# Performance work log

Hardware: AMD Instinct MI355X
Metric: run time of the kernel (lower is better)

Reference implementation:

```python
import jax, jax.numpy as jnp
import numpy as np

D, T, B, DEPTH, WIN, H = 1024, 2048, 4, 2, 128, 4
HD = D // H


def setup_inputs() -> dict:
    key = jax.random.key(0)
    ks = iter(jax.random.split(key, 32))
    s = D ** -0.5
    inp = {
        'x': jax.random.normal(next(ks), (B, T, D), jnp.float32),
        'ln1_s': jnp.ones((DEPTH, D)), 'ln1_b': jnp.zeros((DEPTH, D)),
        'ln2_s': jnp.ones((DEPTH, D)), 'ln2_b': jnp.zeros((DEPTH, D)),
        'ln3_s': jnp.ones((DEPTH, D)), 'ln3_b': jnp.zeros((DEPTH, D)),
        'rg_in_w': jax.random.normal(next(ks), (DEPTH, D, D)) * s,
        'rg_in_b': jnp.zeros((DEPTH, D)),
        'rg_gate_w': jax.random.normal(next(ks), (DEPTH, D, D)) * s,
        'rg_gate_b': jnp.zeros((DEPTH, D)),
        'rg_out_w': jax.random.normal(next(ks), (DEPTH, D, D)) * s,
        'rg_out_b': jnp.zeros((DEPTH, D)),
        'qkv_w': jax.random.normal(next(ks), (DEPTH, D, 3 * D)) * s,
        'qkv_b': jnp.zeros((DEPTH, 3 * D)),
        'attn_out_w': jax.random.normal(next(ks), (DEPTH, D, D)) * s,
        'attn_out_b': jnp.zeros((DEPTH, D)),
        'mlp_w1': jax.random.normal(next(ks), (DEPTH, D, 4 * D)) * s,
        'mlp_b1': jnp.zeros((DEPTH, 4 * D)),
        'mlp_w2': jax.random.normal(next(ks), (DEPTH, 4 * D, D)) * (4 * D) ** -0.5,
        'mlp_b2': jnp.zeros((DEPTH, D)),
    }
    return inp


def _ln(x, s, b):
    m = x.mean(-1, keepdims=True)
    v = ((x - m) ** 2).mean(-1, keepdims=True)
    return (x - m) / jnp.sqrt(v + 1e-5) * s + b


def _rg_lru(x, wi, bi, wg, bg, wo, bo):
    u = x @ wi + bi                      # [B,T,D]
    g = jax.nn.sigmoid(x @ wg + bg)      # [B,T,D]
    # h_t = g_t * h_{t-1} + (1-g_t) * u_t, h_{-1}=0 -> log-depth associative scan
    def comb(l, r):
        return (l[0] * r[0], r[0] * l[1] + r[1])
    _, h = jax.lax.associative_scan(comb, (g, (1.0 - g) * u), axis=1)
    return h @ wo + bo


def _local_attn(x, wqkv, bqkv, wo, bo):
    b, t, d = x.shape
    qkv = (x @ wqkv + bqkv).reshape(b, t, 3, H, HD)
    qkv = jnp.transpose(qkv, (2, 0, 3, 1, 4))  # [3,B,H,T,hd]
    q, k, v = qkv[0], qkv[1], qkv[2]
    scores = jnp.einsum('bhid,bhjd->bhij', q, k) / (HD ** 0.5)
    i = jnp.arange(t)[:, None]
    j = jnp.arange(t)[None, :]
    mask = (j <= i) & (j >= i - (WIN - 1))
    scores = jnp.where(mask, scores, -jnp.inf)
    p = jax.nn.softmax(scores, axis=-1)
    y = jnp.einsum('bhij,bhjd->bhid', p, v)
    y = jnp.transpose(y, (0, 2, 1, 3)).reshape(b, t, d)
    return y @ wo + bo


def reference(x, ln1_s, ln1_b, ln2_s, ln2_b, ln3_s, ln3_b,
              rg_in_w, rg_in_b, rg_gate_w, rg_gate_b, rg_out_w, rg_out_b,
              qkv_w, qkv_b, attn_out_w, attn_out_b,
              mlp_w1, mlp_b1, mlp_w2, mlp_b2):
    for l in range(DEPTH):
        x = x + _rg_lru(_ln(x, ln1_s[l], ln1_b[l]),
                        rg_in_w[l], rg_in_b[l], rg_gate_w[l], rg_gate_b[l],
                        rg_out_w[l], rg_out_b[l])
        x = x + _local_attn(_ln(x, ln2_s[l], ln2_b[l]),
                            qkv_w[l], qkv_b[l], attn_out_w[l], attn_out_b[l])
        h = _ln(x, ln3_s[l], ln3_b[l])
        h = jax.nn.gelu(h @ mlp_w1[l] + mlp_b1[l], approximate=False) @ mlp_w2[l] + mlp_b2[l]
        x = x + h
    return x
```

## Files before the change

### kernel.cpp

```cpp
#include <hip/hip_runtime.h>
#include <math.h>

#define DD 1024
#define TT 2048
#define BB 4
#define HH 4
#define HDIM 256
#define NLAYER 2
#define MM (BB*TT)
#define NCHUNK 32
#define CHUNK (TT/NCHUNK)

typedef unsigned short u16;
typedef __bf16 bf16x8 __attribute__((ext_vector_type(8)));
typedef float f32x4 __attribute__((ext_vector_type(4)));

__device__ __forceinline__ float b2f(u16 h) {
  unsigned u = ((unsigned)h) << 16;
  return __builtin_bit_cast(float, u);
}
__device__ __forceinline__ u16 f2b(float f) {
  unsigned u = __builtin_bit_cast(unsigned, f);
  u += 0x7fffu + ((u >> 16) & 1u);
  return (u16)(u >> 16);
}
__device__ __forceinline__ float blo(unsigned u) { return __builtin_bit_cast(float, u << 16); }
__device__ __forceinline__ float bhi(unsigned u) { return __builtin_bit_cast(float, u & 0xffff0000u); }

#define GLD16(g, l) __builtin_amdgcn_global_load_lds( \
    (__attribute__((address_space(1))) void*)(void*)(g), \
    (__attribute__((address_space(3))) void*)(l), 16, 0, 0)

__device__ __forceinline__ void wg_barrier() {
  asm volatile("" ::: "memory");
  __builtin_amdgcn_s_barrier();
  asm volatile("" ::: "memory");
}

__global__ __launch_bounds__(256)
void transpose_cvt(const float* __restrict__ W, u16* __restrict__ Wt, int K, int N) {
  __shared__ float tile[32][33];
  const int n0 = blockIdx.x << 5, k0 = blockIdx.y << 5;
  const int tx = threadIdx.x, ty = threadIdx.y;
#pragma unroll
  for (int i = 0; i < 4; ++i)
    tile[ty + i*8][tx] = W[(size_t)(k0 + ty + i*8) * N + n0 + tx];
  __syncthreads();
#pragma unroll
  for (int i = 0; i < 4; ++i)
    Wt[(size_t)(n0 + ty + i*8) * K + k0 + tx] = f2b(tile[tx][ty + i*8]);
}

__global__ __launch_bounds__(256)
void ln_k(const float* __restrict__ x, const float* __restrict__ sc,
          const float* __restrict__ bi, u16* __restrict__ xn) {
  const int row = blockIdx.x;
  const int tid = threadIdx.x;
  const float4 xv = ((const float4*)(x + (size_t)row * DD))[tid];
  float s = xv.x + xv.y + xv.z + xv.w;
  float q = xv.x*xv.x + xv.y*xv.y + xv.z*xv.z + xv.w*xv.w;
#pragma unroll
  for (int o = 1; o < 64; o <<= 1) { s += __shfl_xor(s, o); q += __shfl_xor(q, o); }
  __shared__ float rs[4], rq[4];
  if ((tid & 63) == 0) { rs[tid >> 6] = s; rq[tid >> 6] = q; }
  __syncthreads();
  s = rs[0] + rs[1] + rs[2] + rs[3];
  q = rq[0] + rq[1] + rq[2] + rq[3];
  const float mean = s * (1.f / DD);
  const float var = q * (1.f / DD) - mean * mean;
  const float rstd = rsqrtf(var + 1e-5f);
  const float4 sv = ((const float4*)sc)[tid];
  const float4 bv = ((const float4*)bi)[tid];
  const u16 o0 = f2b((xv.x - mean) * rstd * sv.x + bv.x);
  const u16 o1 = f2b((xv.y - mean) * rstd * sv.y + bv.y);
  const u16 o2 = f2b((xv.z - mean) * rstd * sv.z + bv.z);
  const u16 o3 = f2b((xv.w - mean) * rstd * sv.w + bv.w);
  uint2 pk;
  pk.x = (unsigned)o0 | ((unsigned)o1 << 16);
  pk.y = (unsigned)o2 | ((unsigned)o3 << 16);
  *(uint2*)(xn + (size_t)row * DD + (tid << 2)) = pk;
}

template<int EPI>
__global__ __launch_bounds__(256)
void gemm_k(const u16* __restrict__ A, const u16* __restrict__ Wt,
            const float* __restrict__ bias, const float* __restrict__ bias2,
            float* __restrict__ outf, float* __restrict__ outf2,
            u16* __restrict__ outb, int K, int N) {
  __shared__ u16 As[2][8192];
  __shared__ u16 Bs[2][8192];
  const int tid = threadIdx.x;
  const int gx = gridDim.x;
  const int nwg = gx * (int)gridDim.y;
  int lid = (int)blockIdx.y * gx + (int)blockIdx.x;
  lid = (lid & 7) * (nwg >> 3) + (lid >> 3);
  const int m0 = (lid / gx) << 7;
  const int n0 = (lid % gx) << 7;
  const int lane = tid & 63;
  const int wm = (tid >> 7) & 1;
  const int wn = (tid >> 6) & 1;
  const int g = lane >> 4;
  const int lc = lane & 15;
  const int sw = lc & 7;
  const int rowst = tid >> 3;
  const int aslot = (tid & 7) ^ (rowst & 7);

  const u16* Abase = A  + (size_t)m0 * K;
  const u16* Bbase = Wt + (size_t)n0 * K;

  auto stage = [&](int kt, int buf) {
    const int ko = (kt << 6) + (aslot << 3);
#pragma unroll
    for (int i = 0; i < 4; ++i) {
      GLD16(Abase + (size_t)(i*32 + rowst) * K + ko, As[buf] + (i*256 + tid)*8);
      GLD16(Bbase + (size_t)(i*32 + rowst) * K + ko, Bs[buf] + (i*256 + tid)*8);
    }
  };

  f32x4 acc[4][4];
#pragma unroll
  for (int i = 0; i < 4; ++i)
#pragma unroll
    for (int j = 0; j < 4; ++j)
#pragma unroll
      for (int e = 0; e < 4; ++e) acc[i][j][e] = 0.f;

  const int KT = K >> 6;
  stage(0, 0);
  stage(1, 1);
  for (int kt = 0; kt < KT; ++kt) {
    const int cur = kt & 1;
    if (kt + 1 < KT) asm volatile("s_waitcnt vmcnt(8)" ::: "memory");
    else             asm volatile("s_waitcnt vmcnt(0)" ::: "memory");
    __builtin_amdgcn_s_barrier();
    asm volatile("" ::: "memory");
    const u16* Ac = As[cur];
    const u16* Bc = Bs[cur];
#pragma unroll
    for (int kk = 0; kk < 2; ++kk) {
      const int ko = ((kk*4 + g) ^ sw) << 3;
      bf16x8 af[4], bfr[4];
#pragma unroll
      for (int mi = 0; mi < 4; ++mi)
        af[mi] = *(const bf16x8*)(Ac + ((wm*64 + mi*16 + lc) << 6) + ko);
#pragma unroll
      for (int ni = 0; ni < 4; ++ni)
        bfr[ni] = *(const bf16x8*)(Bc + ((wn*64 + ni*16 + lc) << 6) + ko);
      __builtin_amdgcn_s_setprio(1);
#pragma unroll
      for (int mi = 0; mi < 4; ++mi)
#pragma unroll
        for (int ni = 0; ni < 4; ++ni)
          acc[mi][ni] = __builtin_amdgcn_mfma_f32_16x16x32_bf16(af[mi], bfr[ni], acc[mi][ni], 0, 0, 0);
      __builtin_amdgcn_s_setprio(0);
    }
    wg_barrier();
    if (kt + 2 < KT) stage(kt + 2, cur);
  }

#pragma unroll
  for (int mi = 0; mi < 4; ++mi) {
#pragma unroll
    for (int ni = 0; ni < 4; ++ni) {
      const int n = n0 + (wn << 6) + ni*16 + lc;
      const int mbase = m0 + (wm << 6) + mi*16 + (g << 2);
      if (EPI == 4) {
        const float bia = bias[n];
        if (n < 2048) {
#pragma unroll
          for (int e = 0; e < 4; ++e)
            outb[(size_t)(mbase + e) * 2048 + n] = f2b(acc[mi][ni][e] + bia);
        } else {
          const int hh = (n - 2048) >> 8, dim = (n - 2048) & 255;
          const int bidx = mbase >> 11, t = mbase & 2047;
          const u16 a0 = f2b(acc[mi][ni][0] + bia);
          const u16 a1 = f2b(acc[mi][ni][1] + bia);
          const u16 a2 = f2b(acc[mi][ni][2] + bia);
          const u16 a3 = f2b(acc[mi][ni][3] + bia);
          uint2 pk;
          pk.x = (unsigned)a0 | ((unsigned)a1 << 16);
          pk.y = (unsigned)a2 | ((unsigned)a3 << 16);
          u16* vtp = (u16*)outf;
          *(uint2*)(vtp + ((size_t)((bidx*4 + hh)*256 + dim)) * 2048 + t) = pk;
        }
      } else if (EPI == 5) {
        const float bia = (n < 1024) ? bias[n] : bias2[n - 1024];
        u16* dst = (n < 1024) ? (u16*)outf : (u16*)outf2;
        const int nn = n & 1023;
#pragma unroll
        for (int e = 0; e < 4; ++e)
          dst[(size_t)(mbase + e) * 1024 + nn] = f2b(acc[mi][ni][e] + bia);
      } else {
        const float bia = bias[n];
#pragma unroll
        for (int e = 0; e < 4; ++e) {
          const float v = acc[mi][ni][e] + bia;
          const size_t idx = (size_t)(mbase + e) * N + n;
          if (EPI == 2) {
            const float zc = fminf(fmaxf(1.5957691216f * (v + 0.044715f*v*v*v), -30.f), 30.f);
            outb[idx] = f2b(v / (1.f + __expf(-zc)));
          } else outf[idx] += v;
        }
      }
    }
  }
}

__global__ __launch_bounds__(256)
void scan1_k(const u16* __restrict__ zpre, const u16* __restrict__ u,
             float* __restrict__ aggA, float* __restrict__ aggB) {
  const int d = blockIdx.x * 256 + threadIdx.x;
  const int c = blockIdx.y, b = blockIdx.z;
  const size_t base = ((size_t)b * TT + (size_t)c * CHUNK) * DD + d;
  float a = 1.f, acc = 0.f;
  for (int t = 0; t < CHUNK; ++t) {
    const float gl = 1.f / (1.f + __expf(-b2f(zpre[base + (size_t)t * DD])));
    const float ul = b2f(u[base + (size_t)t * DD]);
    acc = gl * acc + (1.f - gl) * ul;
    a *= gl;
  }
  const size_t o = ((size_t)b * NCHUNK + c) * DD + d;
  aggA[o] = a; aggB[o] = acc;
}

__global__ __launch_bounds__(256)
void scan2_k(const float* __restrict__ aggA, const float* __restrict__ aggB,
             float* __restrict__ carry) {
  const int idx = blockIdx.x * 256 + threadIdx.x;
  const int b = idx >> 10, d = idx & 1023;
  float h = 0.f;
  for (int c = 0; c < NCHUNK; ++c) {
    const size_t o = ((size_t)b * NCHUNK + c) * DD + d;
    carry[o] = h;
    h = aggA[o] * h + aggB[o];
  }
}

__global__ __launch_bounds__(256)
void scan3_k(const u16* __restrict__ zpre, const u16* __restrict__ u,
             const float* __restrict__ carry, u16* __restrict__ hout) {
  const int d = blockIdx.x * 256 + threadIdx.x;
  const int c = blockIdx.y, b = blockIdx.z;
  const size_t base = ((size_t)b * TT + (size_t)c * CHUNK) * DD + d;
  float h = carry[((size_t)b * NCHUNK + c) * DD + d];
  for (int t = 0; t < CHUNK; ++t) {
    const float gl = 1.f / (1.f + __expf(-b2f(zpre[base + (size_t)t * DD])));
    const float ul = b2f(u[base + (size_t)t * DD]);
    h = gl * h + (1.f - gl) * ul;
    hout[base + (size_t)t * DD] = f2b(h);
  }
}

__global__ __launch_bounds__(256)
void attn_mfma(const u16* __restrict__ qkb, const u16* __restrict__ vt,
               u16* __restrict__ y) {
  __shared__ u16 kv[16384];
  __shared__ u16 pb[4][16][200];
  const int tid = threadIdx.x;
  const int lane = tid & 63;
  const int wid = tid >> 6;
  const int g = lane >> 4;
  const int lc = lane & 15;
  const int t0 = blockIdx.x << 6;
  const int bh = blockIdx.y;
  const int bT = (bh >> 2) * TT;
  const int h = bh & 3;

  bf16x8 afq[8];
  {
    const u16* qg = qkb + (size_t)(bT + t0 + wid*16 + lc) * 2048 + h*256 + g*8;
#pragma unroll
    for (int ks = 0; ks < 8; ++ks)
      afq[ks] = __builtin_bit_cast(bf16x8, *(const uint4*)(qg + ks*32));
  }

  f32x4 sc[12];
#pragma unroll
  for (int f = 0; f < 12; ++f)
#pragma unroll
    for (int e = 0; e < 4; ++e) sc[f][e] = 0.f;

  const int koff = 1024 + h*256;
#pragma unroll
  for (int c = 0; c < 3; ++c) {
    const int j0 = t0 + (c - 2) * 64;
    if (j0 < 0) {
#pragma unroll
      for (int nt = 0; nt < 4; ++nt)
#pragma unroll
        for (int e = 0; e < 4; ++e) sc[c*4+nt][e] = -1e30f;
      continue;
    }
    __syncthreads();
    {
      const u16* kg = qkb + (size_t)(bT + j0) * 2048 + koff;
#pragma unroll
      for (int i = 0; i < 8; ++i) {
        const int o16 = i*256 + tid;
        const int slab = o16 >> 8, key = (o16 >> 2) & 63, ds = o16 & 3;
        GLD16(kg + (size_t)key*2048 + slab*32 + ds*8, kv + o16*8);
      }
    }
    __syncthreads();
#pragma unroll
    for (int nt = 0; nt < 4; ++nt) {
      f32x4 s = sc[c*4+nt];
#pragma unroll
      for (int ks = 0; ks < 8; ++ks) {
        const bf16x8 kb = *(const bf16x8*)(kv + ks*2048 + (nt*16 + lc)*32 + g*8);
        s = __builtin_amdgcn_mfma_f32_16x16x32_bf16(afq[ks], kb, s, 0, 0, 0);
      }
      sc[c*4+nt] = s;
    }
#pragma unroll
    for (int nt = 0; nt < 4; ++nt)
#pragma unroll
      for (int e = 0; e < 4; ++e) {
        const int tl = wid*16 + g*4 + e;
        const int jl = nt*16 + lc;
        const bool ok = (c == 1) || (c == 2 ? (jl <= tl) : (jl >= tl + 1));
        sc[c*4+nt][e] = ok ? sc[c*4+nt][e] * 0.0625f : -1e30f;
      }
  }

#pragma unroll
  for (int e = 0; e < 4; ++e) {
    float m = -1e30f;
#pragma unroll
    for (int f = 0; f < 12; ++f) m = fmaxf(m, sc[f][e]);
    m = fmaxf(m, __shfl_xor(m, 1)); m = fmaxf(m, __shfl_xor(m, 2));
    m = fmaxf(m, __shfl_xor(m, 4)); m = fmaxf(m, __shfl_xor(m, 8));
    float s = 0.f;
#pragma unroll
    for (int f = 0; f < 12; ++f) { const float p = __expf(sc[f][e] - m); sc[f][e] = p; s += p; }
    s += __shfl_xor(s, 1); s += __shfl_xor(s, 2);
    s += __shfl_xor(s, 4); s += __shfl_xor(s, 8);
    const float is = 1.f / s;
#pragma unroll
    for (int f = 0; f < 12; ++f) sc[f][e] *= is;
  }
#pragma unroll
  for (int c = 0; c < 3; ++c)
#pragma unroll
    for (int nt = 0; nt < 4; ++nt)
#pragma unroll
      for (int e = 0; e < 4; ++e)
        pb[wid][g*4 + e][c*64 + nt*16 + lc] = f2b(sc[c*4+nt][e]);

  f32x4 acc[16];
#pragma unroll
  for (int nt = 0; nt < 16; ++nt)
#pragma unroll
    for (int e = 0; e < 4; ++e) acc[nt][e] = 0.f;

  const u16* vg = vt + (size_t)bh * 256 * 2048;
#pragma unroll
  for (int c = 0; c < 3; ++c) {
    const int j0 = t0 + (c - 2) * 64;
    if (j0 < 0) continue;
    __syncthreads();
#pragma unroll
    for (int i = 0; i < 8; ++i) {
      const int o16 = i*256 + tid;
      const int dim = o16 >> 3, slot = o16 & 7;
      const int ss = slot ^ (dim & 7);
      GLD16(vg + (size_t)dim*2048 + j0 + ss*8, kv + o16*8);
    }
    __syncthreads();
#pragma unroll
    for (int ks = 0; ks < 2; ++ks) {
      const bf16x8 pa = *(const bf16x8*)&pb[wid][lc][(c*2 + ks)*32 + g*8];
#pragma unroll
      for (int nt = 0; nt < 16; ++nt) {
        const int dim = nt*16 + lc;
        int boff = dim*128 + ks*64 + g*16;
        boff ^= (dim & 7) << 4;
        const bf16x8 vb = *(const bf16x8*)((const char*)kv + boff);
        acc[nt] = __builtin_amdgcn_mfma_f32_16x16x32_bf16(pa, vb, acc[nt], 0, 0, 0);
      }
    }
  }

#pragma unroll
  for (int nt = 0; nt < 16; ++nt)
#pragma unroll
    for (int e = 0; e < 4; ++e) {
      const int tok = bT + t0 + wid*16 + g*4 + e;
      y[(size_t)tok * 1024 + h*256 + nt*16 + lc] = f2b(acc[nt][e]);
    }
}

extern "C" void kernel_launch(void* const* d_in, const int* in_sizes, int n_in,
                              void* d_out, int out_size, void* d_ws, size_t ws_size,
                              hipStream_t stream) {
  const float* x_in      = (const float*)d_in[0];
  const float* ln1_s     = (const float*)d_in[1];
  const float* ln1_b     = (const float*)d_in[2];
  const float* ln2_s     = (const float*)d_in[3];
  const float* ln2_b     = (const float*)d_in[4];
  const float* ln3_s     = (const float*)d_in[5];
  const float* ln3_b     = (const float*)d_in[6];
  const float* rg_in_w   = (const float*)d_in[7];
  const float* rg_in_b   = (const float*)d_in[8];
  const float* rg_gate_w = (const float*)d_in[9];
  const float* rg_gate_b = (const float*)d_in[10];
  const float* rg_out_w  = (const float*)d_in[11];
  const float* rg_out_b  = (const float*)d_in[12];
  const float* qkv_w     = (const float*)d_in[13];
  const float* qkv_b     = (const float*)d_in[14];
  const float* attn_out_w= (const float*)d_in[15];
  const float* attn_out_b= (const float*)d_in[16];
  const float* mlp_w1    = (const float*)d_in[17];
  const float* mlp_b1    = (const float*)d_in[18];
  const float* mlp_w2    = (const float*)d_in[19];
  const float* mlp_b2    = (const float*)d_in[20];

  float* x = (float*)d_out;
  char* ws = (char*)d_ws;
  u16*  wt     = (u16*)ws;
  u16*  xn     = (u16*)(ws + 62914560);
  char* bigS   = ws + 62914560 + 16777216;
  char* smallS = bigS + 67108864;
  float* aggA  = (float*)(smallS + 16777216);
  float* aggB  = aggA + (size_t)BB * NCHUNK * DD;
  float* carry = aggB + (size_t)BB * NCHUNK * DD;

  u16* ubuf = (u16*)bigS;
  u16* zbuf = (u16*)(bigS + 33554432);
  u16* qkb  = (u16*)bigS;
  u16* vtb  = (u16*)(bigS + 33554432);
  u16* hid  = (u16*)bigS;
  u16* hbuf = (u16*)smallS;
  u16* ybuf = (u16*)smallS;

  hipMemcpyAsync(x, x_in, (size_t)MM * DD * sizeof(float), hipMemcpyDeviceToDevice, stream);

  const size_t LW = 15728640;
  const dim3 tb(32, 8);
  for (int l = 0; l < NLAYER; ++l) {
    u16* base = wt + (size_t)l * LW;
    transpose_cvt<<<dim3(32, 32),  tb, 0, stream>>>(rg_in_w   + (size_t)l*DD*DD,   base + 0,        DD, DD);
    transpose_cvt<<<dim3(32, 32),  tb, 0, stream>>>(rg_gate_w + (size_t)l*DD*DD,   base + 1048576,  DD, DD);
    transpose_cvt<<<dim3(32, 32),  tb, 0, stream>>>(rg_out_w  + (size_t)l*DD*DD,   base + 2097152,  DD, DD);
    transpose_cvt<<<dim3(96, 32),  tb, 0, stream>>>(qkv_w     + (size_t)l*DD*3072, base + 3145728,  DD, 3072);
    transpose_cvt<<<dim3(32, 32),  tb, 0, stream>>>(attn_out_w+ (size_t)l*DD*DD,   base + 6291456,  DD, DD);
    transpose_cvt<<<dim3(128, 32), tb, 0, stream>>>(mlp_w1    + (size_t)l*DD*4096, base + 7340032,  DD, 4096);
    transpose_cvt<<<dim3(32, 128), tb, 0, stream>>>(mlp_w2    + (size_t)l*4096*DD, base + 11534336, 4096, DD);
  }

  for (int l = 0; l < NLAYER; ++l) {
    u16* base = wt + (size_t)l * LW;
    ln_k<<<MM, 256, 0, stream>>>(x, ln1_s + l*DD, ln1_b + l*DD, xn);
    gemm_k<5><<<dim3(16, 64), 256, 0, stream>>>(xn, base + 0, rg_in_b + l*DD, rg_gate_b + l*DD,
                                                (float*)ubuf, (float*)zbuf, nullptr, DD, 2048);
    scan1_k<<<dim3(4, NCHUNK, BB), 256, 0, stream>>>(zbuf, ubuf, aggA, aggB);
    scan2_k<<<16, 256, 0, stream>>>(aggA, aggB, carry);
    scan3_k<<<dim3(4, NCHUNK, BB), 256, 0, stream>>>(zbuf, ubuf, carry, hbuf);
    gemm_k<3><<<dim3(8, 64), 256, 0, stream>>>(hbuf, base + 2097152, rg_out_b + l*DD, nullptr,
                                               x, nullptr, nullptr, DD, DD);
    ln_k<<<MM, 256, 0, stream>>>(x, ln2_s + l*DD, ln2_b + l*DD, xn);
    gemm_k<4><<<dim3(24, 64), 256, 0, stream>>>(xn, base + 3145728, qkv_b + l*3072, nullptr,
                                                (float*)vtb, nullptr, qkb, DD, 3072);
    attn_mfma<<<dim3(TT/64, BB*HH), 256, 0, stream>>>(qkb, vtb, ybuf);
    gemm_k<3><<<dim3(8, 64), 256, 0, stream>>>(ybuf, base + 6291456, attn_out_b + l*DD, nullptr,
                                               x, nullptr, nullptr, DD, DD);
    ln_k<<<MM, 256, 0, stream>>>(x, ln3_s + l*DD, ln3_b + l*DD, xn);
    gemm_k<2><<<dim3(32, 64), 256, 0, stream>>>(xn, base + 7340032, mlp_b1 + l*4096, nullptr,
                                                nullptr, nullptr, hid, DD, 4096);
    gemm_k<3><<<dim3(8, 64), 256, 0, stream>>>(hid, base + 11534336, mlp_b2 + l*DD, nullptr,
                                               x, nullptr, nullptr, 4096, DD);
  }
}
```

Before: 945.4 us.

## Add 256x256-tile GEMM kernel with 8 waves for wide-N projections

Adds a new 512-thread GEMM kernel with 256x256 output tiles and 128KB of dynamic LDS. Global loads of the next K-tile are split into four parts and interleaved with the MFMA sub-steps of the current tile. It is used for the wide projections (RG-LRU in/gate, QKV, MLP up). The goal is higher arithmetic intensity and less global/L2 traffic per FLOP than the 128x128 kernel. In exchange it uses more registers and LDS, has fewer workgroups per CU, and launches fewer tiles, which can hurt occupancy and wave balance on 256 CUs.

```diff
diff --git a/kernel.cpp b/kernel.cpp
--- a/kernel.cpp
+++ b/kernel.cpp
@@ -82,11 +82,144 @@
 }
 
 template<int EPI>
+__global__ __launch_bounds__(512, 2)
+void gemm256_k(const u16* __restrict__ A, const u16* __restrict__ Wt,
+               const float* __restrict__ bias, const float* __restrict__ bias2,
+               float* __restrict__ outf, u16* __restrict__ outb, int K, int N) {
+  extern __shared__ u16 lds[];
+  u16* Al = lds;
+  u16* Bl = lds + 32768;
+  const int tid = threadIdx.x;
+  const int gx = gridDim.x;
+  const int nwg = gx * (int)gridDim.y;
+  int lid = (int)blockIdx.y * gx + (int)blockIdx.x;
+  lid = (lid & 7) * (nwg >> 3) + (lid >> 3);
+  const int m0 = (lid / gx) << 8;
+  const int n0 = (lid % gx) << 8;
+  const int lane = tid & 63;
+  const int wid = tid >> 6;
+  const int wm = wid >> 2;
+  const int wn = wid & 3;
+  const int g = lane >> 4;
+  const int lc = lane & 15;
+
+  const int srow = tid >> 3;
+  const int sslot = tid & 7;
+
+  auto stage_part = [&](int kt, int c, int p) {
+    if (p < 2) {
+#pragma unroll
+      for (int i = p*2; i < p*2 + 2; ++i) {
+        const int row = i*64 + srow;
+        GLD16(A + (size_t)(m0 + row) * K + kt*64 + ((sslot ^ (row & 7)) << 3),
+              Al + c*16384 + row*64 + sslot*8);
+      }
+    } else {
+#pragma unroll
+      for (int i = (p-2)*2; i < (p-2)*2 + 2; ++i) {
+        const int row = i*64 + srow;
+        GLD16(Wt + (size_t)(n0 + row) * K + kt*64 + ((sslot ^ (row & 7)) << 3),
+              Bl + c*16384 + row*64 + sslot*8);
+      }
+    }
+  };
+
+  f32x4 acc[8][4];
+#pragma unroll
+  for (int i = 0; i < 8; ++i)
+#pragma unroll
+    for (int j = 0; j < 4; ++j)
+#pragma unroll
+      for (int e = 0; e < 4; ++e) acc[i][j][e] = 0.f;
+
+  const int KT = K >> 6;
+#pragma unroll
+  for (int p = 0; p < 4; ++p) stage_part(0, 0, p);
+
+  for (int kt = 0; kt < KT; ++kt) {
+    const int cur = kt & 1;
+    asm volatile("s_waitcnt vmcnt(0)" ::: "memory");
+    wg_barrier();
+    bf16x8 bfr[4];
+#pragma unroll
+    for (int p = 0; p < 4; ++p) {
+      const int kk = p >> 1, mh = p & 1;
+      const int c16 = ((kk*4 + g) ^ (lc & 7)) << 3;
+      bf16x8 af[4];
+#pragma unroll
+      for (int i = 0; i < 4; ++i) {
+        const int row = wm*128 + (mh*4 + i)*16 + lc;
+        af[i] = *(const bf16x8*)(Al + cur*16384 + row*64 + c16);
+      }
+      if (mh == 0) {
+#pragma unroll
+        for (int ni = 0; ni < 4; ++ni) {
+          const int row = wn*64 + ni*16 + lc;
+          bfr[ni] = *(const bf16x8*)(Bl + cur*16384 + row*64 + c16);
+        }
+      }
+      if (kt + 1 < KT) stage_part(kt + 1, cur ^ 1, p);
+      wg_barrier();
+      __builtin_amdgcn_s_setprio(1);
+#pragma unroll
+      for (int i = 0; i < 4; ++i)
+#pragma unroll
+        for (int ni = 0; ni < 4; ++ni)
+          acc[mh*4 + i][ni] = __builtin_amdgcn_mfma_f32_16x16x32_bf16(af[i], bfr[ni], acc[mh*4 + i][ni], 0, 0, 0);
+      __builtin_amdgcn_s_setprio(0);
+      wg_barrier();
+    }
+  }
+
+#pragma unroll
+  for (int mi = 0; mi < 8; ++mi) {
+#pragma unroll
+    for (int ni = 0; ni < 4; ++ni) {
+      const int n = n0 + wn*64 + ni*16 + lc;
+      const int mbase = m0 + wm*128 + mi*16 + (g << 2);
+      if (EPI == 4) {
+        const float bia = bias[n];
+        if (n < 2048) {
+#pragma unroll
+          for (int e = 0; e < 4; ++e)
+            outb[(size_t)(mbase + e) * 2048 + n] = f2b(acc[mi][ni][e] + bia);
+        } else {
+          const int hh = (n - 2048) >> 8, dim = (n - 2048) & 255;
+          const int bidx = mbase >> 11, t = mbase & 2047;
+          const u16 a0 = f2b(acc[mi][ni][0] + bia);
+          const u16 a1 = f2b(acc[mi][ni][1] + bia);
+          const u16 a2 = f2b(acc[mi][ni][2] + bia);
+          const u16 a3 = f2b(acc[mi][ni][3] + bia);
+          uint2 pk;
+          pk.x = (unsigned)a0 | ((unsigned)a1 << 16);
+          pk.y = (unsigned)a2 | ((unsigned)a3 << 16);
+          u16* vtp = (u16*)outf;
+          *(uint2*)(vtp + ((size_t)((bidx*4 + hh)*256 + dim)) * 2048 + t) = pk;
+        }
+      } else if (EPI == 5) {
+        const float bia = (n < 1024) ? bias[n] : bias2[n - 1024];
+        u16* dst = (n < 1024) ? outb : (u16*)outf;
+        const int nn = n & 1023;
+#pragma unroll
+        for (int e = 0; e < 4; ++e)
+          dst[(size_t)(mbase + e) * 1024 + nn] = f2b(acc[mi][ni][e] + bia);
+      } else {
+        const float bia = bias[n];
+#pragma unroll
+        for (int e = 0; e < 4; ++e) {
+          const float v = acc[mi][ni][e] + bia;
+          const float zc = fminf(fmaxf(1.5957691216f * (v + 0.044715f*v*v*v), -30.f), 30.f);
+          outb[(size_t)(mbase + e) * N + n] = f2b(v / (1.f + __expf(-zc)));
+        }
+      }
+    }
+  }
+}
+
+template<int EPI>
 __global__ __launch_bounds__(256)
 void gemm_k(const u16* __restrict__ A, const u16* __restrict__ Wt,
-            const float* __restrict__ bias, const float* __restrict__ bias2,
-            float* __restrict__ outf, float* __restrict__ outf2,
-            u16* __restrict__ outb, int K, int N) {
+            const float* __restrict__ bias, float* __restrict__ outf, int K, int N) {
   __shared__ u16 As[2][8192];
   __shared__ u16 Bs[2][8192];
   const int tid = threadIdx.x;
@@ -164,44 +297,10 @@
     for (int ni = 0; ni < 4; ++ni) {
       const int n = n0 + (wn << 6) + ni*16 + lc;
       const int mbase = m0 + (wm << 6) + mi*16 + (g << 2);
-      if (EPI == 4) {
-        const float bia = bias[n];
-        if (n < 2048) {
-#pragma unroll
-          for (int e = 0; e < 4; ++e)
-            outb[(size_t)(mbase + e) * 2048 + n] = f2b(acc[mi][ni][e] + bia);
-        } else {
-          const int hh = (n - 2048) >> 8, dim = (n - 2048) & 255;
-          const int bidx = mbase >> 11, t = mbase & 2047;
-          const u16 a0 = f2b(acc[mi][ni][0] + bia);
-          const u16 a1 = f2b(acc[mi][ni][1] + bia);
-          const u16 a2 = f2b(acc[mi][ni][2] + bia);
-          const u16 a3 = f2b(acc[mi][ni][3] + bia);
-          uint2 pk;
-          pk.x = (unsigned)a0 | ((unsigned)a1 << 16);
-          pk.y = (unsigned)a2 | ((unsigned)a3 << 16);
-          u16* vtp = (u16*)outf;
-          *(uint2*)(vtp + ((size_t)((bidx*4 + hh)*256 + dim)) * 2048 + t) = pk;
-        }
-      } else if (EPI == 5) {
-        const float bia = (n < 1024) ? bias[n] : bias2[n - 1024];
-        u16* dst = (n < 1024) ? (u16*)outf : (u16*)outf2;
-        const int nn = n & 1023;
-#pragma unroll
-        for (int e = 0; e < 4; ++e)
-          dst[(size_t)(mbase + e) * 1024 + nn] = f2b(acc[mi][ni][e] + bia);
-      } else {
-        const float bia = bias[n];
-#pragma unroll
-        for (int e = 0; e < 4; ++e) {
-          const float v = acc[mi][ni][e] + bia;
-          const size_t idx = (size_t)(mbase + e) * N + n;
-          if (EPI == 2) {
-            const float zc = fminf(fmaxf(1.5957691216f * (v + 0.044715f*v*v*v), -30.f), 30.f);
-            outb[idx] = f2b(v / (1.f + __expf(-zc)));
-          } else outf[idx] += v;
-        }
-      }
+      const float bia = bias[n];
+#pragma unroll
+      for (int e = 0; e < 4; ++e)
+        outf[(size_t)(mbase + e) * N + n] += acc[mi][ni][e] + bia;
     }
   }
 }
@@ -415,6 +514,10 @@
   const float* mlp_w2    = (const float*)d_in[19];
   const float* mlp_b2    = (const float*)d_in[20];
 
+  hipFuncSetAttribute((const void*)&gemm256_k<5>, hipFuncAttributeMaxDynamicSharedMemorySize, 131072);
+  hipFuncSetAttribute((const void*)&gemm256_k<4>, hipFuncAttributeMaxDynamicSharedMemorySize, 131072);
+  hipFuncSetAttribute((const void*)&gemm256_k<2>, hipFuncAttributeMaxDynamicSharedMemorySize, 131072);
+
   float* x = (float*)d_out;
   char* ws = (char*)d_ws;
   u16*  wt     = (u16*)ws;
@@ -451,23 +554,20 @@
   for (int l = 0; l < NLAYER; ++l) {
     u16* base = wt + (size_t)l * LW;
     ln_k<<<MM, 256, 0, stream>>>(x, ln1_s + l*DD, ln1_b + l*DD, xn);
-    gemm_k<5><<<dim3(16, 64), 256, 0, stream>>>(xn, base + 0, rg_in_b + l*DD, rg_gate_b + l*DD,
-                                                (float*)ubuf, (float*)zbuf, nullptr, DD, 2048);
+    gemm256_k<5><<<dim3(8, 32), 512, 131072, stream>>>(xn, base + 0, rg_in_b + l*DD, rg_gate_b + l*DD,
+                                                       (float*)zbuf, ubuf, DD, 2048);
     scan1_k<<<dim3(4, NCHUNK, BB), 256, 0, stream>>>(zbuf, ubuf, aggA, aggB);
     scan2_k<<<16, 256, 0, stream>>>(aggA, aggB, carry);
     scan3_k<<<dim3(4, NCHUNK, BB), 256, 0, stream>>>(zbuf, ubuf, carry, hbuf);
-    gemm_k<3><<<dim3(8, 64), 256, 0, stream>>>(hbuf, base + 2097152, rg_out_b + l*DD, nullptr,
-                                               x, nullptr, nullptr, DD, DD);
+    gemm_k<3><<<dim3(8, 64), 256, 0, stream>>>(hbuf, base + 2097152, rg_out_b + l*DD, x, DD, DD);
     ln_k<<<MM, 256, 0, stream>>>(x, ln2_s + l*DD, ln2_b + l*DD, xn);
-    gemm_k<4><<<dim3(24, 64), 256, 0, stream>>>(xn, base + 3145728, qkv_b + l*3072, nullptr,
-                                                (float*)vtb, nullptr, qkb, DD, 3072);
+    gemm256_k<4><<<dim3(12, 32), 512, 131072, stream>>>(xn, base + 3145728, qkv_b + l*3072, nullptr,
+                                                        (float*)vtb, qkb, DD, 3072);
     attn_mfma<<<dim3(TT/64, BB*HH), 256, 0, stream>>>(qkb, vtb, ybuf);
-    gemm_k<3><<<dim3(8, 64), 256, 0, stream>>>(ybuf, base + 6291456, attn_out_b + l*DD, nullptr,
-                                               x, nullptr, nullptr, DD, DD);
+    gemm_k<3><<<dim3(8, 64), 256, 0, stream>>>(ybuf, base + 6291456, attn_out_b + l*DD, x, DD, DD);
     ln_k<<<MM, 256, 0, stream>>>(x, ln3_s + l*DD, ln3_b + l*DD, xn);
-    gemm_k<2><<<dim3(32, 64), 256, 0, stream>>>(xn, base + 7340032, mlp_b1 + l*4096, nullptr,
-                                                nullptr, nullptr, hid, DD, 4096);
-    gemm_k<3><<<dim3(8, 64), 256, 0, stream>>>(hid, base + 11534336, mlp_b2 + l*DD, nullptr,
-                                               x, nullptr, nullptr, 4096, DD);
-  }
-}
+    gemm256_k<2><<<dim3(16, 32), 512, 131072, stream>>>(xn, base + 7340032, mlp_b1 + l*4096, nullptr,
+                                                        nullptr, hid, DD, 4096);
+    gemm_k<3><<<dim3(8, 64), 256, 0, stream>>>(hid, base + 11534336, mlp_b2 + l*DD, x, 4096, DD);
+  }
+}
```

Result: faster. 920.3 us (-2.6%).

## Replace 128x128 GEMM with 256-row, 512-thread tiles and split-K staging

Applied to the files above, without the earlier changes.

Swaps the 128x128 bf16 MFMA GEMM for a 256xBN tile (BN 256 or 128) run by 8 waves, using dynamic LDS up to 128KB. Each 64-wide k-step is staged as two 32-wide halves, and the next tile's loads are issued mid-iteration instead of keeping a fixed two-ahead prefetch. The aim is more reuse per LDS load and fewer blocks. In exchange it needs more registers and LDS per block, which lowers occupancy, and leaves small grids (256 blocks) for the N=1024 GEMMs.

```diff
diff --git a/kernel.cpp b/kernel.cpp
--- a/kernel.cpp
+++ b/kernel.cpp
@@ -24,8 +24,6 @@
   u += 0x7fffu + ((u >> 16) & 1u);
   return (u16)(u >> 16);
 }
-__device__ __forceinline__ float blo(unsigned u) { return __builtin_bit_cast(float, u << 16); }
-__device__ __forceinline__ float bhi(unsigned u) { return __builtin_bit_cast(float, u & 0xffff0000u); }
 
 #define GLD16(g, l) __builtin_amdgcn_global_load_lds( \
     (__attribute__((address_space(1))) void*)(void*)(g), \
@@ -35,6 +33,9 @@
   asm volatile("" ::: "memory");
   __builtin_amdgcn_s_barrier();
   asm volatile("" ::: "memory");
+}
+template<int N> __device__ __forceinline__ void wait_vmcnt() {
+  asm volatile("s_waitcnt vmcnt(%0)" :: "i"(N) : "memory");
 }
 
 __global__ __launch_bounds__(256)
@@ -81,89 +82,112 @@
   *(uint2*)(xn + (size_t)row * DD + (tid << 2)) = pk;
 }
 
-template<int EPI>
-__global__ __launch_bounds__(256)
-void gemm_k(const u16* __restrict__ A, const u16* __restrict__ Wt,
-            const float* __restrict__ bias, const float* __restrict__ bias2,
-            float* __restrict__ outf, float* __restrict__ outf2,
-            u16* __restrict__ outb, int K, int N) {
-  __shared__ u16 As[2][8192];
-  __shared__ u16 Bs[2][8192];
+template<int EPI, int BN>
+__global__ __launch_bounds__(512)
+void gemm256t(const u16* __restrict__ A, const u16* __restrict__ Wt,
+              const float* __restrict__ bias, const float* __restrict__ bias2,
+              float* __restrict__ outf, u16* __restrict__ outb, int K, int N) {
+  constexpr int NI = BN / 64;
+  constexpr int PAIR = 2 + BN / 128;
+  extern __shared__ u16 lds[];
+  u16* Al = lds;
+  u16* Bl = lds + 32768;
   const int tid = threadIdx.x;
   const int gx = gridDim.x;
   const int nwg = gx * (int)gridDim.y;
   int lid = (int)blockIdx.y * gx + (int)blockIdx.x;
   lid = (lid & 7) * (nwg >> 3) + (lid >> 3);
-  const int m0 = (lid / gx) << 7;
-  const int n0 = (lid % gx) << 7;
+  const int m0 = (lid / gx) << 8;
+  const int n0 = (lid % gx) * BN;
   const int lane = tid & 63;
-  const int wm = (tid >> 7) & 1;
-  const int wn = (tid >> 6) & 1;
+  const int wid = tid >> 6;
+  const int wm = wid >> 2;
+  const int wn = wid & 3;
   const int g = lane >> 4;
   const int lc = lane & 15;
-  const int sw = lc & 7;
-  const int rowst = tid >> 3;
-  const int aslot = (tid & 7) ^ (rowst & 7);
-
-  const u16* Abase = A  + (size_t)m0 * K;
-  const u16* Bbase = Wt + (size_t)n0 * K;
-
-  auto stage = [&](int kt, int buf) {
-    const int ko = (kt << 6) + (aslot << 3);
-#pragma unroll
-    for (int i = 0; i < 4; ++i) {
-      GLD16(Abase + (size_t)(i*32 + rowst) * K + ko, As[buf] + (i*256 + tid)*8);
-      GLD16(Bbase + (size_t)(i*32 + rowst) * K + ko, Bs[buf] + (i*256 + tid)*8);
+  const int rkey = (lc >> 1) & 3;
+  const int q = tid >> 2;
+  const int sslot = tid & 3;
+  const int skey = (q >> 1) & 3;
+  const int scs = (sslot ^ skey) << 3;
+
+  auto stage_pair = [&](int kt, int buf, int ch) {
+    const int kbase = (kt << 6) + (ch << 5);
+#pragma unroll
+    for (int i = 0; i < 2; ++i) {
+      const int row = i*128 + q;
+      GLD16(A + (size_t)(m0 + row) * K + kbase + scs,
+            Al + buf*16384 + ch*8192 + i*4096 + tid*8);
+    }
+#pragma unroll
+    for (int i = 0; i < BN/128; ++i) {
+      const int row = i*128 + q;
+      GLD16(Wt + (size_t)(n0 + row) * K + kbase + scs,
+            Bl + buf*(BN*64) + ch*(BN*32) + i*4096 + tid*8);
     }
   };
 
-  f32x4 acc[4][4];
-#pragma unroll
-  for (int i = 0; i < 4; ++i)
-#pragma unroll
-    for (int j = 0; j < 4; ++j)
+  f32x4 acc[8][NI];
+#pragma unroll
+  for (int i = 0; i < 8; ++i)
+#pragma unroll
+    for (int j = 0; j < NI; ++j)
 #pragma unroll
       for (int e = 0; e < 4; ++e) acc[i][j][e] = 0.f;
 
   const int KT = K >> 6;
-  stage(0, 0);
-  stage(1, 1);
+  stage_pair(0, 0, 0);
+  stage_pair(0, 0, 1);
+
   for (int kt = 0; kt < KT; ++kt) {
     const int cur = kt & 1;
-    if (kt + 1 < KT) asm volatile("s_waitcnt vmcnt(8)" ::: "memory");
-    else             asm volatile("s_waitcnt vmcnt(0)" ::: "memory");
-    __builtin_amdgcn_s_barrier();
-    asm volatile("" ::: "memory");
-    const u16* Ac = As[cur];
-    const u16* Bc = Bs[cur];
+    const bool more = (kt + 1 < KT);
 #pragma unroll
     for (int kk = 0; kk < 2; ++kk) {
-      const int ko = ((kk*4 + g) ^ sw) << 3;
-      bf16x8 af[4], bfr[4];
-#pragma unroll
-      for (int mi = 0; mi < 4; ++mi)
-        af[mi] = *(const bf16x8*)(Ac + ((wm*64 + mi*16 + lc) << 6) + ko);
-#pragma unroll
-      for (int ni = 0; ni < 4; ++ni)
-        bfr[ni] = *(const bf16x8*)(Bc + ((wn*64 + ni*16 + lc) << 6) + ko);
+      if (kk == 0) wait_vmcnt<PAIR>();
+      else if (more) wait_vmcnt<PAIR>();
+      else wait_vmcnt<0>();
+      wg_barrier();
+      const int so = (g ^ rkey) << 3;
+      const u16* Ab = Al + cur*16384 + kk*8192;
+      const u16* Bb = Bl + cur*(BN*64) + kk*(BN*32);
+      bf16x8 bfr[NI];
+#pragma unroll
+      for (int ni = 0; ni < NI; ++ni)
+        bfr[ni] = *(const bf16x8*)(Bb + (wn*(NI*16) + ni*16 + lc)*32 + so);
+      bf16x8 af0[4];
+#pragma unroll
+      for (int i = 0; i < 4; ++i)
+        af0[i] = *(const bf16x8*)(Ab + (wm*128 + i*16 + lc)*32 + so);
+      if (more) stage_pair(kt + 1, cur ^ 1, kk);
       __builtin_amdgcn_s_setprio(1);
 #pragma unroll
-      for (int mi = 0; mi < 4; ++mi)
-#pragma unroll
-        for (int ni = 0; ni < 4; ++ni)
-          acc[mi][ni] = __builtin_amdgcn_mfma_f32_16x16x32_bf16(af[mi], bfr[ni], acc[mi][ni], 0, 0, 0);
+      for (int i = 0; i < 4; ++i)
+#pragma unroll
+        for (int ni = 0; ni < NI; ++ni)
+          acc[i][ni] = __builtin_amdgcn_mfma_f32_16x16x32_bf16(af0[i], bfr[ni], acc[i][ni], 0, 0, 0);
       __builtin_amdgcn_s_setprio(0);
+      bf16x8 af1[4];
+#pragma unroll
+      for (int i = 0; i < 4; ++i)
+        af1[i] = *(const bf16x8*)(Ab + (wm*128 + 64 + i*16 + lc)*32 + so);
+      __builtin_amdgcn_s_setprio(1);
+#pragma unroll
+      for (int i = 0; i < 4; ++i)
+#pragma unroll
+        for (int ni = 0; ni < NI; ++ni)
+          acc[4 + i][ni] = __builtin_amdgcn_mfma_f32_16x16x32_bf16(af1[i], bfr[ni], acc[4 + i][ni], 0, 0, 0);
+      __builtin_amdgcn_s_setprio(0);
     }
     wg_barrier();
-    if (kt + 2 < KT) stage(kt + 2, cur);
-  }
-
-#pragma unroll
-  for (int mi = 0; mi < 4; ++mi) {
-#pragma unroll
-    for (int ni = 0; ni < 4; ++ni) {
-      const int n = n0 + (wn << 6) + ni*16 + lc;
-      const int mbase = m0 + (wm << 6) + mi*16 + (g << 2);
+  }
+
+#pragma unroll
+  for (int mi = 0; mi < 8; ++mi) {
+#pragma unroll
+    for (int ni = 0; ni < NI; ++ni) {
+      const int n = n0 + wn*(NI*16) + ni*16 + lc;
+      const int mbase = m0 + wm*128 + (mi & 3)*16 + (mi >> 2)*64 + (g << 2);
       if (EPI == 4) {
         const float bia = bias[n];
         if (n < 2048) {
@@ -185,22 +209,24 @@
         }
       } else if (EPI == 5) {
         const float bia = (n < 1024) ? bias[n] : bias2[n - 1024];
-        u16* dst = (n < 1024) ? (u16*)outf : (u16*)outf2;
+        u16* dst = (n < 1024) ? outb : (u16*)outf;
         const int nn = n & 1023;
 #pragma unroll
         for (int e = 0; e < 4; ++e)
           dst[(size_t)(mbase + e) * 1024 + nn] = f2b(acc[mi][ni][e] + bia);
+      } else if (EPI == 2) {
+        const float bia = bias[n];
+#pragma unroll
+        for (int e = 0; e < 4; ++e) {
+          const float v = acc[mi][ni][e] + bia;
+          const float zc = fminf(fmaxf(1.5957691216f * (v + 0.044715f*v*v*v), -30.f), 30.f);
+          outb[(size_t)(mbase + e) * N + n] = f2b(v / (1.f + __expf(-zc)));
+        }
       } else {
         const float bia = bias[n];
 #pragma unroll
-        for (int e = 0; e < 4; ++e) {
-          const float v = acc[mi][ni][e] + bia;
-          const size_t idx = (size_t)(mbase + e) * N + n;
-          if (EPI == 2) {
-            const float zc = fminf(fmaxf(1.5957691216f * (v + 0.044715f*v*v*v), -30.f), 30.f);
-            outb[idx] = f2b(v / (1.f + __expf(-zc)));
-          } else outf[idx] += v;
-        }
+        for (int e = 0; e < 4; ++e)
+          outf[(size_t)(mbase + e) * N + n] += acc[mi][ni][e] + bia;
       }
     }
   }
@@ -415,6 +441,11 @@
   const float* mlp_w2    = (const float*)d_in[19];
   const float* mlp_b2    = (const float*)d_in[20];
 
+  hipFuncSetAttribute((const void*)&gemm256t<5,256>, hipFuncAttributeMaxDynamicSharedMemorySize, 131072);
+  hipFuncSetAttribute((const void*)&gemm256t<4,256>, hipFuncAttributeMaxDynamicSharedMemorySize, 131072);
+  hipFuncSetAttribute((const void*)&gemm256t<2,256>, hipFuncAttributeMaxDynamicSharedMemorySize, 131072);
+  hipFuncSetAttribute((const void*)&gemm256t<3,128>, hipFuncAttributeMaxDynamicSharedMemorySize, 98304);
+
   float* x = (float*)d_out;
   char* ws = (char*)d_ws;
   u16*  wt     = (u16*)ws;
@@ -451,23 +482,23 @@
   for (int l = 0; l < NLAYER; ++l) {
     u16* base = wt + (size_t)l * LW;
     ln_k<<<MM, 256, 0, stream>>>(x, ln1_s + l*DD, ln1_b + l*DD, xn);
-    gemm_k<5><<<dim3(16, 64), 256, 0, stream>>>(xn, base + 0, rg_in_b + l*DD, rg_gate_b + l*DD,
-                                                (float*)ubuf, (float*)zbuf, nullptr, DD, 2048);
+    gemm256t<5,256><<<dim3(8, 32), 512, 131072, stream>>>(xn, base + 0, rg_in_b + l*DD, rg_gate_b + l*DD,
+                                                          (float*)zbuf, ubuf, DD, 2048);
     scan1_k<<<dim3(4, NCHUNK, BB), 256, 0, stream>>>(zbuf, ubuf, aggA, aggB);
     scan2_k<<<16, 256, 0, stream>>>(aggA, aggB, carry);
     scan3_k<<<dim3(4, NCHUNK, BB), 256, 0, stream>>>(zbuf, ubuf, carry, hbuf);
-    gemm_k<3><<<dim3(8, 64), 256, 0, stream>>>(hbuf, base + 2097152, rg_out_b + l*DD, nullptr,
-                                               x, nullptr, nullptr, DD, DD);
+    gemm256t<3,128><<<dim3(8, 32), 512, 98304, stream>>>(hbuf, base + 2097152, rg_out_b + l*DD, nullptr,
+                                                         x, nullptr, DD, 1024);
     ln_k<<<MM, 256, 0, stream>>>(x, ln2_s + l*DD, ln2_b + l*DD, xn);
-    gemm_k<4><<<dim3(24, 64), 256, 0, stream>>>(xn, base + 3145728, qkv_b + l*3072, nullptr,
-                                                (float*)vtb, nullptr, qkb, DD, 3072);
+    gemm256t<4,256><<<dim3(12, 32), 512, 131072, stream>>>(xn, base + 3145728, qkv_b + l*3072, nullptr,
+                                                           (float*)vtb, qkb, DD, 3072);
     attn_mfma<<<dim3(TT/64, BB*HH), 256, 0, stream>>>(qkb, vtb, ybuf);
-    gemm_k<3><<<dim3(8, 64), 256, 0, stream>>>(ybuf, base + 6291456, attn_out_b + l*DD, nullptr,
-                                               x, nullptr, nullptr, DD, DD);
+    gemm256t<3,128><<<dim3(8, 32), 512, 98304, stream>>>(ybuf, base + 6291456, attn_out_b + l*DD, nullptr,
+                                                         x, nullptr, DD, 1024);
     ln_k<<<MM, 256, 0, stream>>>(x, ln3_s + l*DD, ln3_b + l*DD, xn);
-    gemm_k<2><<<dim3(32, 64), 256, 0, stream>>>(xn, base + 7340032, mlp_b1 + l*4096, nullptr,
-                                                nullptr, nullptr, hid, DD, 4096);
-    gemm_k<3><<<dim3(8, 64), 256, 0, stream>>>(hid, base + 11534336, mlp_b2 + l*DD, nullptr,
-                                               x, nullptr, nullptr, 4096, DD);
-  }
-}
+    gemm256t<2,256><<<dim3(16, 32), 512, 131072, stream>>>(xn, base + 7340032, mlp_b1 + l*4096, nullptr,
+                                                           nullptr, hid, DD, 4096);
+    gemm256t<3,128><<<dim3(8, 32), 512, 98304, stream>>>(hid, base + 11534336, mlp_b2 + l*DD, nullptr,
+                                                         x, nullptr, 4096, 1024);
+  }
+}
```

After: 910.5 us. 1.04x faster.
